# Kernel optimization log

Hardware: AMD Instinct MI355X
Metric: run time of the kernel (lower is better)

Reference implementation:

```python
import jax, jax.numpy as jnp
import numpy as np

N, DIN, H, OUT = 2048, 128, 64, 7


def setup_inputs() -> dict:
    key = jax.random.key(0)
    ks = jax.random.split(key, 24)

    def lin(k, out_d, in_d):
        kw, kb = jax.random.split(k)
        s = 1.0 / np.sqrt(in_d)
        W = jax.random.uniform(kw, (out_d, in_d), minval=-s, maxval=s, dtype=jnp.float32)
        b = jax.random.uniform(kb, (out_d,), minval=-s, maxval=s, dtype=jnp.float32)
        return W, b

    x = jax.random.normal(ks[0], (N, DIN), dtype=jnp.float32)
    A = jax.random.uniform(ks[1], (N, N), dtype=jnp.float32)
    W1, b1 = lin(ks[2], H, DIN)
    WF1, bF1 = lin(ks[3], H, H)
    WF2, bF2 = lin(ks[4], H, H)
    WT1, bT1 = lin(ks[5], H, H)
    WT2, bT2 = lin(ks[6], H, H)
    WC1, bC1 = lin(ks[7], H, H)
    WC2, bC2 = lin(ks[8], H, H)
    Wa, ba = lin(ks[9], H, H)
    q = jax.random.normal(ks[10], (H,), dtype=jnp.float32)
    W2, b2 = lin(ks[11], OUT, H)
    return dict(x=x, A=A, k=4, W1=W1, b1=b1, WF1=WF1, bF1=bF1, WF2=WF2, bF2=bF2,
                WT1=WT1, bT1=bT1, WT2=WT2, bT2=bT2, WC1=WC1, bC1=bC1, WC2=WC2,
                bC2=bC2, Wa=Wa, ba=ba, q=q, W2=W2, b2=b2)


def leaky(x):
    return jnp.where(x > 0, x, 0.1 * x)


def laplacian(A):
    # D^{-1/2} A D^{-1/2} with diagonal D of (rowsum + 1e-10)
    d = (jnp.sum(A, -1) + 1e-10) ** -0.5
    return A * d[:, None] * d[None, :]


def cos_sim(x):
    n = jnp.sqrt(jnp.sum(x * x, -1, keepdims=True))
    s = x / n + 1e-10  # note: +1e-10 AFTER the division, as in the source
    return s @ s.T


def heat(x):
    # exp(-0.5 * sum_d ((x_i - x_j)^2 + 1e-10)); gram trick, same math as
    # the [d, N, N] broadcasted version in the source.
    sq = jnp.sum(x * x, -1)
    dist = sq[:, None] + sq[None, :] - 2.0 * (x @ x.T) + x.shape[-1] * 1e-10
    return jnp.exp(-0.5 * dist)


def l2_norm_rows(x):
    m = jnp.sqrt(jnp.mean(x * x, -1)) + 1e-10
    return x / m[:, None]


def hsic(x1, x2):
    n = x1.shape[-2]
    K1 = x1 @ x1.T
    K2 = x2 @ x2.T
    Rm = jnp.eye(n, dtype=x1.dtype) - jnp.ones((n, n), dtype=x1.dtype) / n
    P = Rm @ K1 @ Rm  # [N, N]
    # mean(I * (P @ K2)) * n^2/(n-1)^2 = trace(P @ K2)/(n-1)^2; K2 symmetric
    return jnp.sum(P * K2) / (n - 1) ** 2


def gnn(z, Ad, W, b):
    return leaky((Ad @ z) @ W.T + b)


def reference(x, A, k, W1, b1, WF1, bF1, WF2, bF2, WT1, bT1, WT2, bT2,
              WC1, bC1, WC2, bC2, Wa, ba, q, W2, b2):
    h = leaky(x @ W1.T + b1)                       # [N, H]
    At = laplacian(A)
    Hh = heat(h)                                    # [N, N]
    rank = jnp.argsort(jnp.argsort(-Hh, axis=-1), axis=-1)  # double-argsort rank
    mask = (rank < k).astype(h.dtype)
    Af = laplacian(cos_sim(h) * mask)
    zf = gnn(gnn(h, Af, WF1, bF1), Af, WF2, bF2)
    zt = gnn(gnn(h, At, WT1, bT1), At, WT2, bT2)
    zcf = gnn(gnn(h, Af, WC1, bC1), Af, WC2, bC2)
    zct = gnn(gnn(h, At, WC1, bC1), At, WC2, bC2)
    Lcf = l2_norm_rows(zcf)
    Lct = l2_norm_rows(zct)
    Lc = jnp.mean((Lcf @ Lcf.T - Lct @ Lct.T) ** 2)
    Ld = hsic(zt, zct) + hsic(zf, zcf)
    zc = (zcf + zct) / 2
    z = jnp.stack([zf, zt, zc], axis=-2)            # [N, 3, H]
    a = jax.nn.softmax(jnp.tanh(z @ Wa.T + ba) @ q, axis=-1)  # [N, 3]
    zagg = jnp.einsum('nkd,nk->nd', z, a)           # [N, H]
    out = zagg @ W2.T + b2                          # [N, OUT]
    return (out, Lc, Ld)
```

## Files before the change

kernel.cpp:

```cpp
#include <hip/hip_runtime.h>
#include <stdint.h>

#define N 2048
#define DIN 128
#define H 64
#define OUTD 7
#define RS 32
#define S1 8
#define S2 8

#define Z_ZT  0
#define Z_ZCT 64
#define Z_ZF  128
#define Z_ZCF 192
#define Z_LCF 256
#define Z_LCT 320

typedef short bf16x8 __attribute__((ext_vector_type(8)));
typedef float floatx4 __attribute__((ext_vector_type(4)));

__device__ __forceinline__ float leaky(float x){ return x > 0.f ? x : 0.1f*x; }

__device__ __forceinline__ unsigned short f2bf(float f){
  unsigned int u = __float_as_uint(f);
  u = u + 0x7FFFu + ((u >> 16) & 1u);
  return (unsigned short)(u >> 16);
}

__device__ __forceinline__ float waveRedSum(float v){
  #pragma unroll
  for (int o = 32; o > 0; o >>= 1) v += __shfl_xor(v, o, 64);
  return v;
}

__device__ __forceinline__ unsigned long long shflx64(unsigned long long v, int m){
  unsigned int lo = (unsigned int)v, hi = (unsigned int)(v >> 32);
  lo = (unsigned int)__shfl_xor((int)lo, m, 64);
  hi = (unsigned int)__shfl_xor((int)hi, m, 64);
  return ((unsigned long long)hi << 32) | lo;
}

__global__ void k_prep(const float* __restrict__ A, float* __restrict__ dA,
                       unsigned short* __restrict__ Abf){
  int i = blockIdx.x;
  const float4* row = (const float4*)(A + (size_t)i * N);
  unsigned short* ob = Abf + (size_t)i * N;
  float s = 0.f;
  #pragma unroll
  for (int it = 0; it < 2; it++){
    int u = threadIdx.x + it*256;
    float4 v = row[u];
    s += v.x + v.y + v.z + v.w;
    ushort4 o;
    o.x = f2bf(v.x); o.y = f2bf(v.y); o.z = f2bf(v.z); o.w = f2bf(v.w);
    *(ushort4*)&ob[u*4] = o;
  }
  __shared__ float red[4];
  s = waveRedSum(s);
  int wid = threadIdx.x >> 6, lane = threadIdx.x & 63;
  if (lane == 0) red[wid] = s;
  __syncthreads();
  if (threadIdx.x == 0){
    float t = red[0] + red[1] + red[2] + red[3];
    dA[i] = 1.0f / sqrtf(t + 1e-10f);
  }
}

__global__ __launch_bounds__(256) void k_h(const float* __restrict__ x,
                    const float* __restrict__ W1g, const float* __restrict__ b1,
                    const float* __restrict__ dA,
                    float* __restrict__ h, unsigned short* __restrict__ hsT,
                    float* __restrict__ sq, float* __restrict__ hsum){
  __shared__ float W1t[DIN][H+1];
  __shared__ float xb[4][DIN];
  __shared__ __align__(16) unsigned short hTb[H][16];
  int tid = threadIdx.x, w = tid >> 6, t = tid & 63;
  int i0 = blockIdx.x * 16;
  for (int u = tid; u < 2048; u += 256){
    float4 g = ((const float4*)W1g)[u];
    int row = u >> 5, c0 = (u & 31) * 4;
    W1t[c0+0][row] = g.x; W1t[c0+1][row] = g.y;
    W1t[c0+2][row] = g.z; W1t[c0+3][row] = g.w;
  }
  __syncthreads();
  float bt = b1[t];
  for (int rr = 0; rr < 4; rr++){
    int i = i0 + w*4 + rr;
    xb[w][t]      = x[(size_t)i*DIN + t];
    xb[w][t + 64] = x[(size_t)i*DIN + t + 64];
    float acc = bt;
    #pragma unroll
    for (int c4 = 0; c4 < DIN/4; c4++){
      float xv[4]; *(float4*)xv = *(const float4*)&xb[w][c4*4];
      acc += xv[0]*W1t[c4*4+0][t] + xv[1]*W1t[c4*4+1][t]
           + xv[2]*W1t[c4*4+2][t] + xv[3]*W1t[c4*4+3][t];
    }
    float hv = leaky(acc);
    h[(size_t)i*H + t] = hv;
    hTb[t][w*4+rr] = f2bf(dA[i]*hv);
    float s2 = waveRedSum(hv*hv);
    float s1 = waveRedSum(hv);
    if (t == 0){ sq[i] = s2; hsum[i] = s1; }
  }
  __syncthreads();
  { int c = tid >> 2, qq = tid & 3;
    ushort4 v = *(ushort4*)&hTb[c][qq*4];
    *(ushort4*)&hsT[(size_t)c*N + i0 + qq*4] = v; }
}

__global__ __launch_bounds__(256) void k_gram(const float* __restrict__ h,
                                              float* __restrict__ DOT){
  __shared__ float at[32][132];
  __shared__ float bt[32][132];
  int bi = blockIdx.x, bj = blockIdx.y;
  int tid = threadIdx.x;
  int rg = tid >> 4, cg = tid & 15;
  float acc[8][8] = {};
  for (int kc = 0; kc < 64; kc += 32){
    for (int u = tid; u < 1024; u += 256){
      int row = u >> 3, k4 = u & 7;
      float4 v = *(const float4*)(h + (size_t)(bi*128 + row)*H + kc + k4*4);
      at[k4*4+0][row] = v.x; at[k4*4+1][row] = v.y;
      at[k4*4+2][row] = v.z; at[k4*4+3][row] = v.w;
    }
    for (int u = tid; u < 1024; u += 256){
      int row = u >> 3, k4 = u & 7;
      float4 v = *(const float4*)(h + (size_t)(bj*128 + row)*H + kc + k4*4);
      bt[k4*4+0][row] = v.x; bt[k4*4+1][row] = v.y;
      bt[k4*4+2][row] = v.z; bt[k4*4+3][row] = v.w;
    }
    __syncthreads();
    for (int k = 0; k < 32; k++){
      float a[8], b[8];
      *(float4*)&a[0] = *(const float4*)&at[k][rg*8];
      *(float4*)&a[4] = *(const float4*)&at[k][rg*8+4];
      *(float4*)&b[0] = *(const float4*)&bt[k][cg*8];
      *(float4*)&b[4] = *(const float4*)&bt[k][cg*8+4];
      #pragma unroll
      for (int ii = 0; ii < 8; ii++)
        #pragma unroll
        for (int jj = 0; jj < 8; jj++)
          acc[ii][jj] += a[ii]*b[jj];
    }
    __syncthreads();
  }
  #pragma unroll
  for (int ii = 0; ii < 8; ii++){
    int r = bi*128 + rg*8 + ii;
    float* out = DOT + (size_t)r*N + bj*128 + cg*8;
    *(float4*)(out)   = make_float4(acc[ii][0], acc[ii][1], acc[ii][2], acc[ii][3]);
    *(float4*)(out+4) = make_float4(acc[ii][4], acc[ii][5], acc[ii][6], acc[ii][7]);
  }
}

__global__ __launch_bounds__(256) void k_topk(const float* __restrict__ DOT,
      const float* __restrict__ sq, const float* __restrict__ hsum,
      int* __restrict__ nidx, float* __restrict__ ncos, float* __restrict__ df){
  int i = blockIdx.x, tid = threadIdx.x;
  __shared__ unsigned long long cand[1024];
  const float4* row = (const float4*)(DOT + (size_t)i * N);
  const float4* sq4 = (const float4*)sq;
  unsigned long long best[4] = {~0ULL, ~0ULL, ~0ULL, ~0ULL};
  #pragma unroll
  for (int blk = 0; blk < 2; blk++){
    int u = tid + blk*256;
    float4 d = row[u];
    float4 s = sq4[u];
    float kv[4] = { s.x - 2.f*d.x, s.y - 2.f*d.y, s.z - 2.f*d.z, s.w - 2.f*d.w };
    #pragma unroll
    for (int e = 0; e < 4; e++){
      unsigned int j = (unsigned int)(u*4 + e);
      unsigned int uk = __float_as_uint(kv[e]);
      uk = (uk & 0x80000000u) ? ~uk : (uk | 0x80000000u);
      unsigned long long c = ((unsigned long long)uk << 32) | j;
      if (c < best[3]){
        best[3] = c;
        unsigned long long t0;
        if (best[3] < best[2]){ t0 = best[2]; best[2] = best[3]; best[3] = t0; }
        if (best[2] < best[1]){ t0 = best[1]; best[1] = best[2]; best[2] = t0; }
        if (best[1] < best[0]){ t0 = best[0]; best[0] = best[1]; best[1] = t0; }
      }
    }
  }
  #pragma unroll
  for (int e = 0; e < 4; e++) cand[e*256 + tid] = best[e];
  __syncthreads();
  if (tid < 64){
    unsigned long long loc[16];
    #pragma unroll
    for (int e = 0; e < 16; e++) loc[e] = cand[e*64 + tid];
    unsigned long long w0=~0ULL, w1=~0ULL, w2=~0ULL, w3=~0ULL;
    #pragma unroll
    for (int r = 0; r < 4; r++){
      unsigned long long m = loc[0];
      #pragma unroll
      for (int e = 1; e < 16; e++) m = (loc[e] < m) ? loc[e] : m;
      unsigned long long g = m;
      #pragma unroll
      for (int o = 32; o > 0; o >>= 1){
        unsigned long long other = shflx64(g, o);
        if (other < g) g = other;
      }
      #pragma unroll
      for (int e = 0; e < 16; e++) if (loc[e] == g) loc[e] = ~0ULL;
      if (r == 0) w0 = g; else if (r == 1) w1 = g; else if (r == 2) w2 = g; else w3 = g;
    }
    float myc = 0.f;
    if (tid < 4){
      unsigned long long w = (tid==0) ? w0 : (tid==1) ? w1 : (tid==2) ? w2 : w3;
      unsigned int j = (unsigned int)w;
      unsigned int uk = (unsigned int)(w >> 32);
      float key = (uk & 0x80000000u) ? __uint_as_float(uk ^ 0x80000000u)
                                     : __uint_as_float(~uk);
      float sqj = sq[j];
      float dot = (sqj - key) * 0.5f;
      float hni = sqrtf(sq[i]), hnj = sqrtf(sqj);
      float cosv = dot/(hni*hnj)
                 + 1e-10f*(hsum[i]/hni + hsum[j]/hnj)
                 + 64.0f*1e-20f;
      nidx[i*4 + tid] = (int)j;
      ncos[i*4 + tid] = cosv;
      myc = cosv;
    }
    myc += __shfl_xor(myc, 1, 64);
    myc += __shfl_xor(myc, 2, 64);
    if (tid == 0) df[i] = 1.f / sqrtf(myc + 1e-10f);
  }
}

template<int BN>
__global__ __launch_bounds__(256) void k_mgemm(
    const unsigned short* __restrict__ Abf, const unsigned short* __restrict__ BtG,
    float* __restrict__ Cp, int KC){
  __shared__ __align__(16) unsigned short Asl[64][72];
  __shared__ __align__(16) unsigned short Bsl[BN][72];
  int m0 = blockIdx.x * 64, kbase = blockIdx.y * KC;
  int tid = threadIdx.x;
  int w = tid >> 6, lane = tid & 63;
  int quad = lane >> 4, ml = lane & 15;
  floatx4 acc[BN/16];
  #pragma unroll
  for (int ct = 0; ct < BN/16; ct++) acc[ct] = (floatx4){0.f,0.f,0.f,0.f};

  for (int kc = 0; kc < KC; kc += 64){
    int kb = kbase + kc;
    #pragma unroll
    for (int u = tid; u < 512; u += 256){
      int r = u >> 3, s = u & 7;
      *(uint4*)&Asl[r][s*8] = *(const uint4*)(Abf + ((size_t)(m0+r) << 11) + kb + s*8);
    }
    #pragma unroll
    for (int u = tid; u < BN*8; u += 256){
      int n = u >> 3, s = u & 7;
      *(uint4*)&Bsl[n][s*8] = *(const uint4*)(BtG + ((size_t)n << 11) + kb + s*8);
    }
    __syncthreads();
    #pragma unroll
    for (int k0 = 0; k0 < 64; k0 += 32){
      bf16x8 af = *(const bf16x8*)&Asl[16*w + ml][k0 + quad*8];
      #pragma unroll
      for (int ct = 0; ct < BN/16; ct++){
        bf16x8 bfr = *(const bf16x8*)&Bsl[16*ct + ml][k0 + quad*8];
        acc[ct] = __builtin_amdgcn_mfma_f32_16x16x32_bf16(af, bfr, acc[ct], 0, 0, 0);
      }
    }
    __syncthreads();
  }
  float* C = Cp + (size_t)blockIdx.y * (N * BN);
  #pragma unroll
  for (int ct = 0; ct < BN/16; ct++)
    #pragma unroll
    for (int r = 0; r < 4; r++){
      int row = m0 + 16*w + quad*4 + r;
      C[(size_t)row*BN + 16*ct + ml] = acc[ct][r];
    }
}

__global__ __launch_bounds__(256) void k_sumY1(const float* __restrict__ Y1p,
    const float* __restrict__ dA, unsigned short* __restrict__ Ub1){
  int idx4 = blockIdx.x*256 + threadIdx.x;
  int i = idx4 >> 4;
  float4 s = ((const float4*)Y1p)[idx4];
  #pragma unroll
  for (int p = 1; p < S1; p++){
    float4 v = ((const float4*)Y1p)[(size_t)p*(N*H/4) + idx4];
    s.x += v.x; s.y += v.y; s.z += v.z; s.w += v.w;
  }
  float d = dA[i];
  ushort4 o;
  o.x = f2bf(s.x*d); o.y = f2bf(s.y*d); o.z = f2bf(s.z*d); o.w = f2bf(s.w*d);
  ((ushort4*)Ub1)[idx4] = o;
}

__global__ __launch_bounds__(256) void k_sumY2(const float* __restrict__ Y2p,
    const float* __restrict__ dA, unsigned short* __restrict__ Ub2){
  int idx4 = blockIdx.x*256 + threadIdx.x;
  int i = idx4 >> 5;
  float4 s = ((const float4*)Y2p)[idx4];
  #pragma unroll
  for (int p = 1; p < S2; p++){
    float4 v = ((const float4*)Y2p)[(size_t)p*(N*128/4) + idx4];
    s.x += v.x; s.y += v.y; s.z += v.z; s.w += v.w;
  }
  float d = dA[i];
  ushort4 o;
  o.x = f2bf(s.x*d); o.y = f2bf(s.y*d); o.z = f2bf(s.z*d); o.w = f2bf(s.w*d);
  ((ushort4*)Ub2)[idx4] = o;
}

__global__ __launch_bounds__(256) void k_gather1(const float* __restrict__ h,
    const int* __restrict__ nidx, const float* __restrict__ ncos,
    const float* __restrict__ df, unsigned short* __restrict__ Vb1){
  int tid = threadIdx.x, w = tid >> 6, t = tid & 63;
  int i = blockIdx.x*4 + w;
  int j0 = nidx[i*4], j1 = nidx[i*4+1], j2 = nidx[i*4+2], j3 = nidx[i*4+3];
  float di = df[i];
  float w0 = ncos[i*4]  *di*df[j0];
  float w1 = ncos[i*4+1]*di*df[j1];
  float w2 = ncos[i*4+2]*di*df[j2];
  float w3 = ncos[i*4+3]*di*df[j3];
  float v = w0*h[(size_t)j0*H+t] + w1*h[(size_t)j1*H+t]
          + w2*h[(size_t)j2*H+t] + w3*h[(size_t)j3*H+t];
  Vb1[(size_t)i*H + t] = f2bf(v);
}

__global__ __launch_bounds__(256) void k_gather2(const float* __restrict__ z1f,
    const float* __restrict__ z1cf,
    const int* __restrict__ nidx, const float* __restrict__ ncos,
    const float* __restrict__ df,
    unsigned short* __restrict__ Vf2, unsigned short* __restrict__ Vc2){
  int tid = threadIdx.x, w = tid >> 6, t = tid & 63;
  int i = blockIdx.x*4 + w;
  int j0 = nidx[i*4], j1 = nidx[i*4+1], j2 = nidx[i*4+2], j3 = nidx[i*4+3];
  float di = df[i];
  float w0 = ncos[i*4]  *di*df[j0];
  float w1 = ncos[i*4+1]*di*df[j1];
  float w2 = ncos[i*4+2]*di*df[j2];
  float w3 = ncos[i*4+3]*di*df[j3];
  float vf = w0*z1f[(size_t)j0*H+t] + w1*z1f[(size_t)j1*H+t]
           + w2*z1f[(size_t)j2*H+t] + w3*z1f[(size_t)j3*H+t];
  float vc = w0*z1cf[(size_t)j0*H+t] + w1*z1cf[(size_t)j1*H+t]
           + w2*z1cf[(size_t)j2*H+t] + w3*z1cf[(size_t)j3*H+t];
  Vf2[(size_t)i*H + t] = f2bf(vf);
  Vc2[(size_t)i*H + t] = f2bf(vc);
}

__global__ __launch_bounds__(256) void k_z1m(
    const unsigned short* __restrict__ Vb1, const unsigned short* __restrict__ Ub1,
    const float* __restrict__ WF1, const float* __restrict__ WC1,
    const float* __restrict__ WT1, const float* __restrict__ bF1,
    const float* __restrict__ bC1, const float* __restrict__ bT1,
    const float* __restrict__ dA,
    float* __restrict__ z1f, float* __restrict__ z1cf,
    unsigned short* __restrict__ ZsT){
  __shared__ __align__(16) unsigned short Vs[64][72];
  __shared__ __align__(16) unsigned short Ws[64][72];
  __shared__ __align__(16) unsigned short Tb[64][72];
  __shared__ float bias[64], dAl[64];
  int p = blockIdx.y, i0 = blockIdx.x * 64, tid = threadIdx.x;
  const unsigned short* Vsrc = (p < 2) ? Vb1 : Ub1;
  const float* Wsrc = (p == 0) ? WF1 : (p == 2) ? WT1 : WC1;
  const float* bsrc = (p == 0) ? bF1 : (p == 2) ? bT1 : bC1;
  #pragma unroll
  for (int u = tid; u < 512; u += 256){
    int r = u >> 3, s = u & 7;
    *(uint4*)&Vs[r][s*8] = *(const uint4*)(Vsrc + (size_t)(i0+r)*H + s*8);
  }
  for (int u = tid; u < 1024; u += 256){
    int r = u >> 4, c4 = (u & 15)*4;
    float4 f = *(const float4*)(Wsrc + (size_t)r*H + c4);
    Ws[r][c4+0] = f2bf(f.x); Ws[r][c4+1] = f2bf(f.y);
    Ws[r][c4+2] = f2bf(f.z); Ws[r][c4+3] = f2bf(f.w);
  }
  if (tid < 64){ bias[tid] = bsrc[tid]; dAl[tid] = dA[i0 + tid]; }
  __syncthreads();
  int w = tid >> 6, lane = tid & 63, quad = lane >> 4, ml = lane & 15;
  floatx4 acc[4];
  #pragma unroll
  for (int ct = 0; ct < 4; ct++) acc[ct] = (floatx4){0.f,0.f,0.f,0.f};
  #pragma unroll
  for (int k0 = 0; k0 < 64; k0 += 32){
    bf16x8 af = *(const bf16x8*)&Vs[16*w + ml][k0 + quad*8];
    #pragma unroll
    for (int ct = 0; ct < 4; ct++){
      bf16x8 bfr = *(const bf16x8*)&Ws[16*ct + ml][k0 + quad*8];
      acc[ct] = __builtin_amdgcn_mfma_f32_16x16x32_bf16(af, bfr, acc[ct], 0, 0, 0);
    }
  }
  if (p < 2){
    float* dst = (p == 0) ? z1f : z1cf;
    #pragma unroll
    for (int ct = 0; ct < 4; ct++){
      int col = 16*ct + ml;
      #pragma unroll
      for (int r = 0; r < 4; r++){
        int row = 16*w + quad*4 + r;
        dst[(size_t)(i0+row)*H + col] = leaky(acc[ct][r] + bias[col]);
      }
    }
  } else {
    #pragma unroll
    for (int ct = 0; ct < 4; ct++){
      int col = 16*ct + ml;
      #pragma unroll
      for (int r = 0; r < 4; r++){
        int row = 16*w + quad*4 + r;
        Tb[col][row] = f2bf(dAl[row] * leaky(acc[ct][r] + bias[col]));
      }
    }
    __syncthreads();
    int zb = (p == 2) ? 0 : 64;
    #pragma unroll
    for (int u = tid; u < 512; u += 256){
      int c = u >> 3, s = u & 7;
      *(uint4*)&ZsT[(size_t)(zb + c)*N + i0 + s*8] = *(uint4*)&Tb[c][s*8];
    }
  }
}

__global__ __launch_bounds__(256) void k_z2m(
    const unsigned short* __restrict__ Vf2, const unsigned short* __restrict__ Vc2,
    const unsigned short* __restrict__ Ub2,
    const float* __restrict__ WF2, const float* __restrict__ WC2,
    const float* __restrict__ WT2, const float* __restrict__ bF2,
    const float* __restrict__ bC2, const float* __restrict__ bT2,
    float* __restrict__ Z6){
  __shared__ __align__(16) unsigned short Vs[64][72];
  __shared__ __align__(16) unsigned short Ws[64][72];
  __shared__ float bias[64];
  int p = blockIdx.y, i0 = blockIdx.x * 64, tid = threadIdx.x;
  const unsigned short* vptr = (p == 0) ? Vf2 : (p == 1) ? Vc2 : Ub2;
  int vstride = (p < 2) ? 64 : 128;
  int voff = (p == 3) ? 64 : 0;
  const float* Wsrc = (p == 0) ? WF2 : (p == 2) ? WT2 : WC2;
  const float* bsrc = (p == 0) ? bF2 : (p == 2) ? bT2 : bC2;
  #pragma unroll
  for (int u = tid; u < 512; u += 256){
    int r = u >> 3, s = u & 7;
    *(uint4*)&Vs[r][s*8] = *(const uint4*)(vptr + (size_t)(i0+r)*vstride + voff + s*8);
  }
  for (int u = tid; u < 1024; u += 256){
    int r = u >> 4, c4 = (u & 15)*4;
    float4 f = *(const float4*)(Wsrc + (size_t)r*H + c4);
    Ws[r][c4+0] = f2bf(f.x); Ws[r][c4+1] = f2bf(f.y);
    Ws[r][c4+2] = f2bf(f.z); Ws[r][c4+3] = f2bf(f.w);
  }
  if (tid < 64) bias[tid] = bsrc[tid];
  __syncthreads();
  int w = tid >> 6, lane = tid & 63, quad = lane >> 4, ml = lane & 15;
  floatx4 acc[4];
  #pragma unroll
  for (int ct = 0; ct < 4; ct++) acc[ct] = (floatx4){0.f,0.f,0.f,0.f};
  #pragma unroll
  for (int k0 = 0; k0 < 64; k0 += 32){
    bf16x8 af = *(const bf16x8*)&Vs[16*w + ml][k0 + quad*8];
    #pragma unroll
    for (int ct = 0; ct < 4; ct++){
      bf16x8 bfr = *(const bf16x8*)&Ws[16*ct + ml][k0 + quad*8];
      acc[ct] = __builtin_amdgcn_mfma_f32_16x16x32_bf16(af, bfr, acc[ct], 0, 0, 0);
    }
  }
  int zoff = (p == 0) ? Z_ZF : (p == 1) ? Z_ZCF : (p == 2) ? Z_ZT : Z_ZCT;
  float val[4][4];
  #pragma unroll
  for (int ct = 0; ct < 4; ct++){
    int col = 16*ct + ml;
    #pragma unroll
    for (int r = 0; r < 4; r++){
      val[ct][r] = leaky(acc[ct][r] + bias[col]);
      int row = 16*w + quad*4 + r;
      Z6[(size_t)(i0+row)*384 + zoff + col] = val[ct][r];
    }
  }
  if (p == 1 || p == 3){
    int loff = (p == 1) ? Z_LCF : Z_LCT;
    #pragma unroll
    for (int r = 0; r < 4; r++){
      float s = val[0][r]*val[0][r] + val[1][r]*val[1][r]
              + val[2][r]*val[2][r] + val[3][r]*val[3][r];
      s += __shfl_xor(s, 1, 64); s += __shfl_xor(s, 2, 64);
      s += __shfl_xor(s, 4, 64); s += __shfl_xor(s, 8, 64);
      float m = sqrtf(s*(1.f/64.f)) + 1e-10f;
      int row = 16*w + quad*4 + r;
      #pragma unroll
      for (int ct = 0; ct < 4; ct++)
        Z6[(size_t)(i0+row)*384 + loff + 16*ct + ml] = val[ct][r]/m;
    }
  }
}

__global__ __launch_bounds__(256) void k_att(const float* __restrict__ Z6,
    const float* __restrict__ Wag, const float* __restrict__ ba,
    const float* __restrict__ q, const float* __restrict__ W2g,
    const float* __restrict__ b2, float* __restrict__ out){
  __shared__ float Wal[64][65];
  __shared__ float W2l[448];
  __shared__ float zbuf[4][3][66];
  __shared__ float zagg[4][66];
  int tid = threadIdx.x, w = tid >> 6, t = tid & 63;
  for (int u = tid; u < 1024; u += 256){
    int r = u >> 4, c4 = (u & 15)*4;
    float4 f = ((const float4*)Wag)[u];
    Wal[r][c4+0]=f.x; Wal[r][c4+1]=f.y; Wal[r][c4+2]=f.z; Wal[r][c4+3]=f.w;
  }
  if (tid < 112) *(float4*)&W2l[tid*4] = ((const float4*)W2g)[tid];
  __syncthreads();
  int i = blockIdx.x*4 + w;
  const float* zr = Z6 + (size_t)i*384;
  float zf = zr[Z_ZF + t], zt = zr[Z_ZT + t];
  float zc = 0.5f*(zr[Z_ZCF + t] + zr[Z_ZCT + t]);
  zbuf[w][0][t] = zf; zbuf[w][1][t] = zt; zbuf[w][2][t] = zc;
  __syncthreads();
  float bav = ba[t], qv = q[t];
  float e[3];
  #pragma unroll
  for (int k = 0; k < 3; k++){
    float S = bav;
    #pragma unroll 8
    for (int c = 0; c < 64; c++) S += zbuf[w][k][c] * Wal[t][c];
    e[k] = waveRedSum(tanhf(S)*qv);
  }
  float mx = fmaxf(e[0], fmaxf(e[1], e[2]));
  float x0 = expf(e[0]-mx), x1 = expf(e[1]-mx), x2 = expf(e[2]-mx);
  float inv = 1.f/(x0+x1+x2);
  zagg[w][t] = x0*inv*zf + x1*inv*zt + x2*inv*zc;
  __syncthreads();
  if (t < OUTD){
    float acc = b2[t];
    #pragma unroll 8
    for (int c = 0; c < 64; c++) acc += zagg[w][c]*W2l[t*64 + c];
    out[(size_t)i*OUTD + t] = acc;
  }
}

__global__ __launch_bounds__(256) void k_reduce(const float* __restrict__ Z6,
                                                float* __restrict__ redP,
                                                float* __restrict__ colP){
  __shared__ float sa[64][68];
  __shared__ float sb[64][68];
  int p = blockIdx.x >> 5;
  int s = blockIdx.x & 31;
  int tid = threadIdx.x;
  const int aoffT[5] = {Z_ZT,  Z_ZF,  Z_LCF, Z_LCF, Z_LCT};
  const int boffT[5] = {Z_ZCT, Z_ZCF, Z_LCF, Z_LCT, Z_LCT};
  int aoff = aoffT[p], boff = boffT[p];
  int r0 = s * 64;
  {
    int row = tid >> 4, c4 = (tid & 15) * 4;
    #pragma unroll
    for (int rr = 0; rr < 64; rr += 16){
      const float* zr = Z6 + (size_t)(r0 + row + rr) * 384;
      *(float4*)&sa[row + rr][c4] = *(const float4*)&zr[aoff + c4];
      *(float4*)&sb[row + rr][c4] = *(const float4*)&zr[boff + c4];
    }
  }
  __syncthreads();
  int rg = tid >> 4, cg = tid & 15;
  float acc[4][4] = {};
  #pragma unroll 8
  for (int k = 0; k < 64; k++){
    float a[4], b[4];
    *(float4*)a = *(const float4*)&sa[k][rg*4];
    *(float4*)b = *(const float4*)&sb[k][cg*4];
    #pragma unroll
    for (int ii = 0; ii < 4; ii++)
      #pragma unroll
      for (int jj = 0; jj < 4; jj++)
        acc[ii][jj] += a[ii]*b[jj];
  }
  float* rp = redP + (size_t)blockIdx.x * 4096;
  #pragma unroll
  for (int ii = 0; ii < 4; ii++)
    *(float4*)&rp[(rg*4+ii)*64 + cg*4] =
      make_float4(acc[ii][0], acc[ii][1], acc[ii][2], acc[ii][3]);
  if (p < 2 && tid < 128){
    int t = tid & 63;
    float csum = 0.f;
    if (tid < 64){
      #pragma unroll 16
      for (int r = 0; r < 64; r++) csum += sa[r][t];
    } else {
      #pragma unroll 16
      for (int r = 0; r < 64; r++) csum += sb[r][t];
    }
    colP[((size_t)p*RS + s)*128 + tid] = csum;
  }
}

__global__ void k_combine(const float* __restrict__ redP,
                          const float* __restrict__ colP,
                          float* __restrict__ red){
  int idx = blockIdx.x*256 + threadIdx.x;
  if (idx < 20480){
    int p = idx >> 12, i = idx & 4095;
    float sum = 0.f;
    #pragma unroll 8
    for (int s = 0; s < RS; s++) sum += redP[((size_t)p*RS + s)*4096 + i];
    red[idx] = sum;
  } else if (idx < 20736){
    int j = idx - 20480;
    int p = j >> 7, rem = j & 127;
    float sum = 0.f;
    #pragma unroll 8
    for (int s = 0; s < RS; s++) sum += colP[((size_t)p*RS + s)*128 + rem];
    red[idx] = sum;
  }
}

__global__ void k_final(const float* __restrict__ red, float* __restrict__ out2){
  int tid = threadIdx.x;
  const float* Stc = red;
  const float* Sfc = red + 4096;
  const float* Cff = red + 8192;
  const float* Cft = red + 12288;
  const float* Ctt = red + 16384;
  const float* cst = red + 20480;
  const float* csct= red + 20544;
  const float* csf = red + 20608;
  const float* cscf= red + 20672;
  float sCff=0, sCft=0, sCtt=0, sM1=0, sM2=0;
  for (int u = tid*16; u < tid*16+16; u++){
    int d = u >> 6, e = u & 63;
    float m1 = Stc[u] - cst[d]*csct[e]*(1.f/2048.f);
    float m2 = Sfc[u] - csf[d]*cscf[e]*(1.f/2048.f);
    sM1 += m1*m1; sM2 += m2*m2;
    float cf = Cff[u], cx = Cft[u], ct = Ctt[u];
    sCff += cf*cf; sCft += cx*cx; sCtt += ct*ct;
  }
  __shared__ float rd[5][4];
  sCff = waveRedSum(sCff); sCft = waveRedSum(sCft); sCtt = waveRedSum(sCtt);
  sM1 = waveRedSum(sM1);   sM2 = waveRedSum(sM2);
  int w = tid >> 6, lane = tid & 63;
  if (lane == 0){ rd[0][w]=sCff; rd[1][w]=sCft; rd[2][w]=sCtt; rd[3][w]=sM1; rd[4][w]=sM2; }
  __syncthreads();
  if (tid == 0){
    float A0 = rd[0][0]+rd[0][1]+rd[0][2]+rd[0][3];
    float A1 = rd[1][0]+rd[1][1]+rd[1][2]+rd[1][3];
    float A2 = rd[2][0]+rd[2][1]+rd[2][2]+rd[2][3];
    float M1 = rd[3][0]+rd[3][1]+rd[3][2]+rd[3][3];
    float M2 = rd[4][0]+rd[4][1]+rd[4][2]+rd[4][3];
    out2[0] = (A0 - 2.f*A1 + A2) * (1.f/(2048.f*2048.f));
    out2[1] = (M1 + M2) * (1.f/(2047.f*2047.f));
  }
}

extern "C" void kernel_launch(void* const* d_in, const int* in_sizes, int n_in,
                              void* d_out, int out_size, void* d_ws, size_t ws_size,
                              hipStream_t stream) {
  const float* x   = (const float*)d_in[0];
  const float* A   = (const float*)d_in[1];
  const float* W1  = (const float*)d_in[3];
  const float* b1  = (const float*)d_in[4];
  const float* WF1 = (const float*)d_in[5];
  const float* bF1 = (const float*)d_in[6];
  const float* WF2 = (const float*)d_in[7];
  const float* bF2 = (const float*)d_in[8];
  const float* WT1 = (const float*)d_in[9];
  const float* bT1 = (const float*)d_in[10];
  const float* WT2 = (const float*)d_in[11];
  const float* bT2 = (const float*)d_in[12];
  const float* WC1 = (const float*)d_in[13];
  const float* bC1 = (const float*)d_in[14];
  const float* WC2 = (const float*)d_in[15];
  const float* bC2 = (const float*)d_in[16];
  const float* Wa  = (const float*)d_in[17];
  const float* ba  = (const float*)d_in[18];
  const float* q   = (const float*)d_in[19];
  const float* W2  = (const float*)d_in[20];
  const float* b2  = (const float*)d_in[21];
  float* out = (float*)d_out;

  float* W = (float*)d_ws;
  float* h_   = W;
  float* dA   = h_  + N*H;
  float* sq   = dA  + N;
  float* hsum = sq  + N;
  float* df   = hsum+ N;
  int*   nidx = (int*)(df + N);
  float* ncos = (float*)(nidx + N*4);
  float* red  = ncos + N*4;
  float* DOT  = red + 20736;
  float* Z6   = DOT + (size_t)N*N;
  float* Y1p  = Z6  + (size_t)N*384;
  float* Y2p  = Y1p + (size_t)S1*N*H;
  float* z1f  = Y2p + (size_t)S2*N*128;
  float* z1cf = z1f + N*H;
  float* redP = z1cf+ N*H;
  float* colP = redP+ 655360;
  unsigned short* Abf = (unsigned short*)(colP + 8192);
  unsigned short* hsT = Abf + (size_t)N*N;
  unsigned short* ZsT = hsT + (size_t)H*N;
  unsigned short* Vb1 = ZsT + (size_t)128*N;
  unsigned short* Ub1 = Vb1 + (size_t)N*H;
  unsigned short* Vf2 = Ub1 + (size_t)N*H;
  unsigned short* Vc2 = Vf2 + (size_t)N*H;
  unsigned short* Ub2 = Vc2 + (size_t)N*H;

  k_prep<<<N, 256, 0, stream>>>(A, dA, Abf);
  k_h<<<128, 256, 0, stream>>>(x, W1, b1, dA, h_, hsT, sq, hsum);
  k_gram<<<dim3(16,16), 256, 0, stream>>>(h_, DOT);
  k_topk<<<N, 256, 0, stream>>>(DOT, sq, hsum, nidx, ncos, df);
  k_gather1<<<512, 256, 0, stream>>>(h_, nidx, ncos, df, Vb1);

  k_mgemm<64><<<dim3(32,S1), 256, 0, stream>>>(Abf, hsT, Y1p, N/S1);
  k_sumY1<<<128, 256, 0, stream>>>(Y1p, dA, Ub1);
  k_z1m<<<dim3(32,4), 256, 0, stream>>>(Vb1, Ub1, WF1, WC1, WT1, bF1, bC1, bT1,
                                        dA, z1f, z1cf, ZsT);
  k_mgemm<128><<<dim3(32,S2), 256, 0, stream>>>(Abf, ZsT, Y2p, N/S2);
  k_sumY2<<<256, 256, 0, stream>>>(Y2p, dA, Ub2);
  k_gather2<<<512, 256, 0, stream>>>(z1f, z1cf, nidx, ncos, df, Vf2, Vc2);
  k_z2m<<<dim3(32,4), 256, 0, stream>>>(Vf2, Vc2, Ub2, WF2, WC2, WT2,
                                        bF2, bC2, bT2, Z6);
  k_att<<<512, 256, 0, stream>>>(Z6, Wa, ba, q, W2, b2, out);
  k_reduce<<<5*RS, 256, 0, stream>>>(Z6, redP, colP);
  k_combine<<<81, 256, 0, stream>>>(redP, colP, red);
  k_final<<<1, 256, 0, stream>>>(red, out + (size_t)N*OUTD);
}
```

Before: 204.1 us.

## Split-bf16 MFMA gram, wave-per-row topk, fuse gathers and split-K sums into z kernels

The fp32 FMA gram kernel is replaced by an MFMA version that splits h into bf16 hi/lo parts and uses three products to keep near-fp32 accuracy. Top-k is restructured so each wave handles one row with a shuffle-based merge, removing the shared-memory candidate stage. The separate gather and split-K reduction kernels are folded into the z1m/z2m GEMM prologues, which removes four launches and their intermediate bf16 buffers. The risks are that the hi/lo approximation could change top-k neighbour choices on near ties, and that the gather in k_z1m now reads bf16 h instead of fp32.

```diff
diff --git a/kernel.cpp b/kernel.cpp
--- a/kernel.cpp
+++ b/kernel.cpp
@@ -27,6 +27,10 @@
   return (unsigned short)(u >> 16);
 }
 
+__device__ __forceinline__ float bf2f(unsigned short u){
+  return __uint_as_float((unsigned int)u << 16);
+}
+
 __device__ __forceinline__ float waveRedSum(float v){
   #pragma unroll
   for (int o = 32; o > 0; o >>= 1) v += __shfl_xor(v, o, 64);
@@ -69,7 +73,9 @@
 __global__ __launch_bounds__(256) void k_h(const float* __restrict__ x,
                     const float* __restrict__ W1g, const float* __restrict__ b1,
                     const float* __restrict__ dA,
-                    float* __restrict__ h, unsigned short* __restrict__ hsT,
+                    unsigned short* __restrict__ hb_hi,
+                    unsigned short* __restrict__ hb_lo,
+                    unsigned short* __restrict__ hsT,
                     float* __restrict__ sq, float* __restrict__ hsum){
   __shared__ float W1t[DIN][H+1];
   __shared__ float xb[4][DIN];
@@ -96,7 +102,9 @@
            + xv[2]*W1t[c4*4+2][t] + xv[3]*W1t[c4*4+3][t];
     }
     float hv = leaky(acc);
-    h[(size_t)i*H + t] = hv;
+    unsigned short hi = f2bf(hv);
+    hb_hi[(size_t)i*H + t] = hi;
+    hb_lo[(size_t)i*H + t] = f2bf(hv - bf2f(hi));
     hTb[t][w*4+rr] = f2bf(dA[i]*hv);
     float s2 = waveRedSum(hv*hv);
     float s1 = waveRedSum(hv);
@@ -108,62 +116,63 @@
     *(ushort4*)&hsT[(size_t)c*N + i0 + qq*4] = v; }
 }
 
-__global__ __launch_bounds__(256) void k_gram(const float* __restrict__ h,
-                                              float* __restrict__ DOT){
-  __shared__ float at[32][132];
-  __shared__ float bt[32][132];
-  int bi = blockIdx.x, bj = blockIdx.y;
-  int tid = threadIdx.x;
-  int rg = tid >> 4, cg = tid & 15;
-  float acc[8][8] = {};
-  for (int kc = 0; kc < 64; kc += 32){
-    for (int u = tid; u < 1024; u += 256){
-      int row = u >> 3, k4 = u & 7;
-      float4 v = *(const float4*)(h + (size_t)(bi*128 + row)*H + kc + k4*4);
-      at[k4*4+0][row] = v.x; at[k4*4+1][row] = v.y;
-      at[k4*4+2][row] = v.z; at[k4*4+3][row] = v.w;
-    }
-    for (int u = tid; u < 1024; u += 256){
-      int row = u >> 3, k4 = u & 7;
-      float4 v = *(const float4*)(h + (size_t)(bj*128 + row)*H + kc + k4*4);
-      bt[k4*4+0][row] = v.x; bt[k4*4+1][row] = v.y;
-      bt[k4*4+2][row] = v.z; bt[k4*4+3][row] = v.w;
-    }
-    __syncthreads();
-    for (int k = 0; k < 32; k++){
-      float a[8], b[8];
-      *(float4*)&a[0] = *(const float4*)&at[k][rg*8];
-      *(float4*)&a[4] = *(const float4*)&at[k][rg*8+4];
-      *(float4*)&b[0] = *(const float4*)&bt[k][cg*8];
-      *(float4*)&b[4] = *(const float4*)&bt[k][cg*8+4];
-      #pragma unroll
-      for (int ii = 0; ii < 8; ii++)
-        #pragma unroll
-        for (int jj = 0; jj < 8; jj++)
-          acc[ii][jj] += a[ii]*b[jj];
-    }
-    __syncthreads();
-  }
-  #pragma unroll
-  for (int ii = 0; ii < 8; ii++){
-    int r = bi*128 + rg*8 + ii;
-    float* out = DOT + (size_t)r*N + bj*128 + cg*8;
-    *(float4*)(out)   = make_float4(acc[ii][0], acc[ii][1], acc[ii][2], acc[ii][3]);
-    *(float4*)(out+4) = make_float4(acc[ii][4], acc[ii][5], acc[ii][6], acc[ii][7]);
-  }
+__global__ __launch_bounds__(256) void k_gram2(
+    const unsigned short* __restrict__ Hhi, const unsigned short* __restrict__ Hlo,
+    float* __restrict__ DOT){
+  __shared__ __align__(16) unsigned short Bh[128][72];
+  __shared__ __align__(16) unsigned short Bl[128][72];
+  int bi = blockIdx.x, bj = blockIdx.y, tid = threadIdx.x;
+  for (int u = tid; u < 1024; u += 256){
+    int r = u >> 3, s = u & 7;
+    *(uint4*)&Bh[r][s*8] = *(const uint4*)(Hhi + (size_t)(bj*128+r)*H + s*8);
+    *(uint4*)&Bl[r][s*8] = *(const uint4*)(Hlo + (size_t)(bj*128+r)*H + s*8);
+  }
+  __syncthreads();
+  int w = tid >> 6, lane = tid & 63, quad = lane >> 4, ml = lane & 15;
+  floatx4 acc[2][8];
+  #pragma unroll
+  for (int rt = 0; rt < 2; rt++)
+    #pragma unroll
+    for (int ct = 0; ct < 8; ct++) acc[rt][ct] = (floatx4){0.f,0.f,0.f,0.f};
+  #pragma unroll
+  for (int rt = 0; rt < 2; rt++){
+    int arow = bi*128 + (2*w + rt)*16 + ml;
+    #pragma unroll
+    for (int k0 = 0; k0 < 64; k0 += 32){
+      bf16x8 ah = *(const bf16x8*)(Hhi + (size_t)arow*H + k0 + quad*8);
+      bf16x8 al = *(const bf16x8*)(Hlo + (size_t)arow*H + k0 + quad*8);
+      #pragma unroll
+      for (int ct = 0; ct < 8; ct++){
+        bf16x8 bh = *(const bf16x8*)&Bh[ct*16 + ml][k0 + quad*8];
+        bf16x8 bl = *(const bf16x8*)&Bl[ct*16 + ml][k0 + quad*8];
+        acc[rt][ct] = __builtin_amdgcn_mfma_f32_16x16x32_bf16(ah, bh, acc[rt][ct], 0,0,0);
+        acc[rt][ct] = __builtin_amdgcn_mfma_f32_16x16x32_bf16(ah, bl, acc[rt][ct], 0,0,0);
+        acc[rt][ct] = __builtin_amdgcn_mfma_f32_16x16x32_bf16(al, bh, acc[rt][ct], 0,0,0);
+      }
+    }
+  }
+  #pragma unroll
+  for (int rt = 0; rt < 2; rt++)
+    #pragma unroll
+    for (int ct = 0; ct < 8; ct++)
+      #pragma unroll
+      for (int r = 0; r < 4; r++){
+        int row = bi*128 + (2*w+rt)*16 + quad*4 + r;
+        DOT[(size_t)row*N + bj*128 + ct*16 + ml] = acc[rt][ct][r];
+      }
 }
 
 __global__ __launch_bounds__(256) void k_topk(const float* __restrict__ DOT,
       const float* __restrict__ sq, const float* __restrict__ hsum,
       int* __restrict__ nidx, float* __restrict__ ncos, float* __restrict__ df){
-  int i = blockIdx.x, tid = threadIdx.x;
-  __shared__ unsigned long long cand[1024];
+  int tid = threadIdx.x, w = tid >> 6, lane = tid & 63;
+  int i = blockIdx.x*4 + w;
   const float4* row = (const float4*)(DOT + (size_t)i * N);
   const float4* sq4 = (const float4*)sq;
   unsigned long long best[4] = {~0ULL, ~0ULL, ~0ULL, ~0ULL};
   #pragma unroll
-  for (int blk = 0; blk < 2; blk++){
-    int u = tid + blk*256;
+  for (int it = 0; it < 8; it++){
+    int u = it*64 + lane;
     float4 d = row[u];
     float4 s = sq4[u];
     float kv[4] = { s.x - 2.f*d.x, s.y - 2.f*d.y, s.z - 2.f*d.z, s.w - 2.f*d.w };
@@ -182,50 +191,41 @@
       }
     }
   }
-  #pragma unroll
-  for (int e = 0; e < 4; e++) cand[e*256 + tid] = best[e];
-  __syncthreads();
-  if (tid < 64){
-    unsigned long long loc[16];
-    #pragma unroll
-    for (int e = 0; e < 16; e++) loc[e] = cand[e*64 + tid];
-    unsigned long long w0=~0ULL, w1=~0ULL, w2=~0ULL, w3=~0ULL;
-    #pragma unroll
-    for (int r = 0; r < 4; r++){
-      unsigned long long m = loc[0];
-      #pragma unroll
-      for (int e = 1; e < 16; e++) m = (loc[e] < m) ? loc[e] : m;
-      unsigned long long g = m;
-      #pragma unroll
-      for (int o = 32; o > 0; o >>= 1){
-        unsigned long long other = shflx64(g, o);
-        if (other < g) g = other;
-      }
-      #pragma unroll
-      for (int e = 0; e < 16; e++) if (loc[e] == g) loc[e] = ~0ULL;
-      if (r == 0) w0 = g; else if (r == 1) w1 = g; else if (r == 2) w2 = g; else w3 = g;
-    }
-    float myc = 0.f;
-    if (tid < 4){
-      unsigned long long w = (tid==0) ? w0 : (tid==1) ? w1 : (tid==2) ? w2 : w3;
-      unsigned int j = (unsigned int)w;
-      unsigned int uk = (unsigned int)(w >> 32);
-      float key = (uk & 0x80000000u) ? __uint_as_float(uk ^ 0x80000000u)
-                                     : __uint_as_float(~uk);
-      float sqj = sq[j];
-      float dot = (sqj - key) * 0.5f;
-      float hni = sqrtf(sq[i]), hnj = sqrtf(sqj);
-      float cosv = dot/(hni*hnj)
-                 + 1e-10f*(hsum[i]/hni + hsum[j]/hnj)
-                 + 64.0f*1e-20f;
-      nidx[i*4 + tid] = (int)j;
-      ncos[i*4 + tid] = cosv;
-      myc = cosv;
-    }
-    myc += __shfl_xor(myc, 1, 64);
-    myc += __shfl_xor(myc, 2, 64);
-    if (tid == 0) df[i] = 1.f / sqrtf(myc + 1e-10f);
-  }
+  unsigned long long win[4];
+  #pragma unroll
+  for (int r = 0; r < 4; r++){
+    unsigned long long m = best[0];
+    #pragma unroll
+    for (int o = 1; o < 64; o <<= 1){
+      unsigned long long other = shflx64(m, o);
+      if (other < m) m = other;
+    }
+    win[r] = m;
+    if      (best[0]==m){best[0]=best[1];best[1]=best[2];best[2]=best[3];best[3]=~0ULL;}
+    else if (best[1]==m){best[1]=best[2];best[2]=best[3];best[3]=~0ULL;}
+    else if (best[2]==m){best[2]=best[3];best[3]=~0ULL;}
+    else if (best[3]==m){best[3]=~0ULL;}
+  }
+  float myc = 0.f;
+  if (lane < 4){
+    unsigned long long wv = win[lane];
+    unsigned int j = (unsigned int)wv;
+    unsigned int uk = (unsigned int)(wv >> 32);
+    float key = (uk & 0x80000000u) ? __uint_as_float(uk ^ 0x80000000u)
+                                   : __uint_as_float(~uk);
+    float sqj = sq[j];
+    float dot = (sqj - key) * 0.5f;
+    float hni = sqrtf(sq[i]), hnj = sqrtf(sqj);
+    float cosv = dot/(hni*hnj)
+               + 1e-10f*(hsum[i]/hni + hsum[j]/hnj)
+               + 64.0f*1e-20f;
+    nidx[i*4 + lane] = (int)j;
+    ncos[i*4 + lane] = cosv;
+    myc = cosv;
+  }
+  myc += __shfl_xor(myc, 1, 64);
+  myc += __shfl_xor(myc, 2, 64);
+  if (lane == 0) df[i] = 1.f / sqrtf(myc + 1e-10f);
 }
 
 template<int BN>
@@ -276,81 +276,14 @@
     }
 }
 
-__global__ __launch_bounds__(256) void k_sumY1(const float* __restrict__ Y1p,
-    const float* __restrict__ dA, unsigned short* __restrict__ Ub1){
-  int idx4 = blockIdx.x*256 + threadIdx.x;
-  int i = idx4 >> 4;
-  float4 s = ((const float4*)Y1p)[idx4];
-  #pragma unroll
-  for (int p = 1; p < S1; p++){
-    float4 v = ((const float4*)Y1p)[(size_t)p*(N*H/4) + idx4];
-    s.x += v.x; s.y += v.y; s.z += v.z; s.w += v.w;
-  }
-  float d = dA[i];
-  ushort4 o;
-  o.x = f2bf(s.x*d); o.y = f2bf(s.y*d); o.z = f2bf(s.z*d); o.w = f2bf(s.w*d);
-  ((ushort4*)Ub1)[idx4] = o;
-}
-
-__global__ __launch_bounds__(256) void k_sumY2(const float* __restrict__ Y2p,
-    const float* __restrict__ dA, unsigned short* __restrict__ Ub2){
-  int idx4 = blockIdx.x*256 + threadIdx.x;
-  int i = idx4 >> 5;
-  float4 s = ((const float4*)Y2p)[idx4];
-  #pragma unroll
-  for (int p = 1; p < S2; p++){
-    float4 v = ((const float4*)Y2p)[(size_t)p*(N*128/4) + idx4];
-    s.x += v.x; s.y += v.y; s.z += v.z; s.w += v.w;
-  }
-  float d = dA[i];
-  ushort4 o;
-  o.x = f2bf(s.x*d); o.y = f2bf(s.y*d); o.z = f2bf(s.z*d); o.w = f2bf(s.w*d);
-  ((ushort4*)Ub2)[idx4] = o;
-}
-
-__global__ __launch_bounds__(256) void k_gather1(const float* __restrict__ h,
-    const int* __restrict__ nidx, const float* __restrict__ ncos,
-    const float* __restrict__ df, unsigned short* __restrict__ Vb1){
-  int tid = threadIdx.x, w = tid >> 6, t = tid & 63;
-  int i = blockIdx.x*4 + w;
-  int j0 = nidx[i*4], j1 = nidx[i*4+1], j2 = nidx[i*4+2], j3 = nidx[i*4+3];
-  float di = df[i];
-  float w0 = ncos[i*4]  *di*df[j0];
-  float w1 = ncos[i*4+1]*di*df[j1];
-  float w2 = ncos[i*4+2]*di*df[j2];
-  float w3 = ncos[i*4+3]*di*df[j3];
-  float v = w0*h[(size_t)j0*H+t] + w1*h[(size_t)j1*H+t]
-          + w2*h[(size_t)j2*H+t] + w3*h[(size_t)j3*H+t];
-  Vb1[(size_t)i*H + t] = f2bf(v);
-}
-
-__global__ __launch_bounds__(256) void k_gather2(const float* __restrict__ z1f,
-    const float* __restrict__ z1cf,
+__global__ __launch_bounds__(256) void k_z1m(
+    const unsigned short* __restrict__ hb,
     const int* __restrict__ nidx, const float* __restrict__ ncos,
     const float* __restrict__ df,
-    unsigned short* __restrict__ Vf2, unsigned short* __restrict__ Vc2){
-  int tid = threadIdx.x, w = tid >> 6, t = tid & 63;
-  int i = blockIdx.x*4 + w;
-  int j0 = nidx[i*4], j1 = nidx[i*4+1], j2 = nidx[i*4+2], j3 = nidx[i*4+3];
-  float di = df[i];
-  float w0 = ncos[i*4]  *di*df[j0];
-  float w1 = ncos[i*4+1]*di*df[j1];
-  float w2 = ncos[i*4+2]*di*df[j2];
-  float w3 = ncos[i*4+3]*di*df[j3];
-  float vf = w0*z1f[(size_t)j0*H+t] + w1*z1f[(size_t)j1*H+t]
-           + w2*z1f[(size_t)j2*H+t] + w3*z1f[(size_t)j3*H+t];
-  float vc = w0*z1cf[(size_t)j0*H+t] + w1*z1cf[(size_t)j1*H+t]
-           + w2*z1cf[(size_t)j2*H+t] + w3*z1cf[(size_t)j3*H+t];
-  Vf2[(size_t)i*H + t] = f2bf(vf);
-  Vc2[(size_t)i*H + t] = f2bf(vc);
-}
-
-__global__ __launch_bounds__(256) void k_z1m(
-    const unsigned short* __restrict__ Vb1, const unsigned short* __restrict__ Ub1,
+    const float* __restrict__ Y1p, const float* __restrict__ dA,
     const float* __restrict__ WF1, const float* __restrict__ WC1,
     const float* __restrict__ WT1, const float* __restrict__ bF1,
     const float* __restrict__ bC1, const float* __restrict__ bT1,
-    const float* __restrict__ dA,
     float* __restrict__ z1f, float* __restrict__ z1cf,
     unsigned short* __restrict__ ZsT){
   __shared__ __align__(16) unsigned short Vs[64][72];
@@ -358,14 +291,9 @@
   __shared__ __align__(16) unsigned short Tb[64][72];
   __shared__ float bias[64], dAl[64];
   int p = blockIdx.y, i0 = blockIdx.x * 64, tid = threadIdx.x;
-  const unsigned short* Vsrc = (p < 2) ? Vb1 : Ub1;
+  int w = tid >> 6, lane = tid & 63;
   const float* Wsrc = (p == 0) ? WF1 : (p == 2) ? WT1 : WC1;
   const float* bsrc = (p == 0) ? bF1 : (p == 2) ? bT1 : bC1;
-  #pragma unroll
-  for (int u = tid; u < 512; u += 256){
-    int r = u >> 3, s = u & 7;
-    *(uint4*)&Vs[r][s*8] = *(const uint4*)(Vsrc + (size_t)(i0+r)*H + s*8);
-  }
   for (int u = tid; u < 1024; u += 256){
     int r = u >> 4, c4 = (u & 15)*4;
     float4 f = *(const float4*)(Wsrc + (size_t)r*H + c4);
@@ -373,8 +301,36 @@
     Ws[r][c4+2] = f2bf(f.z); Ws[r][c4+3] = f2bf(f.w);
   }
   if (tid < 64){ bias[tid] = bsrc[tid]; dAl[tid] = dA[i0 + tid]; }
-  __syncthreads();
-  int w = tid >> 6, lane = tid & 63, quad = lane >> 4, ml = lane & 15;
+  if (p < 2){
+    for (int rr = 0; rr < 16; rr++){
+      int r = w*16 + rr, i = i0 + r;
+      int j0 = nidx[i*4], j1 = nidx[i*4+1], j2 = nidx[i*4+2], j3 = nidx[i*4+3];
+      float di = df[i];
+      float w0 = ncos[i*4]  *di*df[j0];
+      float w1 = ncos[i*4+1]*di*df[j1];
+      float w2 = ncos[i*4+2]*di*df[j2];
+      float w3 = ncos[i*4+3]*di*df[j3];
+      float v = w0*bf2f(hb[(size_t)j0*H+lane]) + w1*bf2f(hb[(size_t)j1*H+lane])
+              + w2*bf2f(hb[(size_t)j2*H+lane]) + w3*bf2f(hb[(size_t)j3*H+lane]);
+      Vs[r][lane] = f2bf(v);
+    }
+  } else {
+    for (int u = tid; u < 1024; u += 256){
+      int r = u >> 4, k4 = u & 15;
+      const float* base = Y1p + (size_t)(i0 + r)*H + k4*4;
+      float4 s = *(const float4*)base;
+      #pragma unroll
+      for (int pp = 1; pp < S1; pp++){
+        float4 v2 = *(const float4*)(base + (size_t)pp*N*H);
+        s.x += v2.x; s.y += v2.y; s.z += v2.z; s.w += v2.w;
+      }
+      float d = dA[i0 + r];
+      Vs[r][k4*4+0] = f2bf(s.x*d); Vs[r][k4*4+1] = f2bf(s.y*d);
+      Vs[r][k4*4+2] = f2bf(s.z*d); Vs[r][k4*4+3] = f2bf(s.w*d);
+    }
+  }
+  __syncthreads();
+  int quad = lane >> 4, ml = lane & 15;
   floatx4 acc[4];
   #pragma unroll
   for (int ct = 0; ct < 4; ct++) acc[ct] = (floatx4){0.f,0.f,0.f,0.f};
@@ -419,8 +375,10 @@
 }
 
 __global__ __launch_bounds__(256) void k_z2m(
-    const unsigned short* __restrict__ Vf2, const unsigned short* __restrict__ Vc2,
-    const unsigned short* __restrict__ Ub2,
+    const float* __restrict__ z1f, const float* __restrict__ z1cf,
+    const int* __restrict__ nidx, const float* __restrict__ ncos,
+    const float* __restrict__ df,
+    const float* __restrict__ Y2p, const float* __restrict__ dA,
     const float* __restrict__ WF2, const float* __restrict__ WC2,
     const float* __restrict__ WT2, const float* __restrict__ bF2,
     const float* __restrict__ bC2, const float* __restrict__ bT2,
@@ -429,16 +387,9 @@
   __shared__ __align__(16) unsigned short Ws[64][72];
   __shared__ float bias[64];
   int p = blockIdx.y, i0 = blockIdx.x * 64, tid = threadIdx.x;
-  const unsigned short* vptr = (p == 0) ? Vf2 : (p == 1) ? Vc2 : Ub2;
-  int vstride = (p < 2) ? 64 : 128;
-  int voff = (p == 3) ? 64 : 0;
+  int w = tid >> 6, lane = tid & 63;
   const float* Wsrc = (p == 0) ? WF2 : (p == 2) ? WT2 : WC2;
   const float* bsrc = (p == 0) ? bF2 : (p == 2) ? bT2 : bC2;
-  #pragma unroll
-  for (int u = tid; u < 512; u += 256){
-    int r = u >> 3, s = u & 7;
-    *(uint4*)&Vs[r][s*8] = *(const uint4*)(vptr + (size_t)(i0+r)*vstride + voff + s*8);
-  }
   for (int u = tid; u < 1024; u += 256){
     int r = u >> 4, c4 = (u & 15)*4;
     float4 f = *(const float4*)(Wsrc + (size_t)r*H + c4);
@@ -446,8 +397,38 @@
     Ws[r][c4+2] = f2bf(f.z); Ws[r][c4+3] = f2bf(f.w);
   }
   if (tid < 64) bias[tid] = bsrc[tid];
-  __syncthreads();
-  int w = tid >> 6, lane = tid & 63, quad = lane >> 4, ml = lane & 15;
+  if (p < 2){
+    const float* src = (p == 0) ? z1f : z1cf;
+    for (int rr = 0; rr < 16; rr++){
+      int r = w*16 + rr, i = i0 + r;
+      int j0 = nidx[i*4], j1 = nidx[i*4+1], j2 = nidx[i*4+2], j3 = nidx[i*4+3];
+      float di = df[i];
+      float w0 = ncos[i*4]  *di*df[j0];
+      float w1 = ncos[i*4+1]*di*df[j1];
+      float w2 = ncos[i*4+2]*di*df[j2];
+      float w3 = ncos[i*4+3]*di*df[j3];
+      float v = w0*src[(size_t)j0*H+lane] + w1*src[(size_t)j1*H+lane]
+              + w2*src[(size_t)j2*H+lane] + w3*src[(size_t)j3*H+lane];
+      Vs[r][lane] = f2bf(v);
+    }
+  } else {
+    int off = (p == 2) ? 0 : 64;
+    for (int u = tid; u < 1024; u += 256){
+      int r = u >> 4, k4 = u & 15;
+      const float* base = Y2p + (size_t)(i0 + r)*128 + off + k4*4;
+      float4 s = *(const float4*)base;
+      #pragma unroll
+      for (int pp = 1; pp < S2; pp++){
+        float4 v2 = *(const float4*)(base + (size_t)pp*N*128);
+        s.x += v2.x; s.y += v2.y; s.z += v2.z; s.w += v2.w;
+      }
+      float d = dA[i0 + r];
+      Vs[r][k4*4+0] = f2bf(s.x*d); Vs[r][k4*4+1] = f2bf(s.y*d);
+      Vs[r][k4*4+2] = f2bf(s.z*d); Vs[r][k4*4+3] = f2bf(s.w*d);
+    }
+  }
+  __syncthreads();
+  int quad = lane >> 4, ml = lane & 15;
   floatx4 acc[4];
   #pragma unroll
   for (int ct = 0; ct < 4; ct++) acc[ct] = (floatx4){0.f,0.f,0.f,0.f};
@@ -671,8 +652,7 @@
   float* out = (float*)d_out;
 
   float* W = (float*)d_ws;
-  float* h_   = W;
-  float* dA   = h_  + N*H;
+  float* dA   = W;
   float* sq   = dA  + N;
   float* hsum = sq  + N;
   float* df   = hsum+ N;
@@ -687,30 +667,24 @@
   float* z1cf = z1f + N*H;
   float* redP = z1cf+ N*H;
   float* colP = redP+ 655360;
-  unsigned short* Abf = (unsigned short*)(colP + 8192);
-  unsigned short* hsT = Abf + (size_t)N*N;
-  unsigned short* ZsT = hsT + (size_t)H*N;
-  unsigned short* Vb1 = ZsT + (size_t)128*N;
-  unsigned short* Ub1 = Vb1 + (size_t)N*H;
-  unsigned short* Vf2 = Ub1 + (size_t)N*H;
-  unsigned short* Vc2 = Vf2 + (size_t)N*H;
-  unsigned short* Ub2 = Vc2 + (size_t)N*H;
+  unsigned short* Abf  = (unsigned short*)(colP + 8192);
+  unsigned short* hsT  = Abf + (size_t)N*N;
+  unsigned short* ZsT  = hsT + (size_t)H*N;
+  unsigned short* hbHi = ZsT + (size_t)128*N;
+  unsigned short* hbLo = hbHi + (size_t)N*H;
 
   k_prep<<<N, 256, 0, stream>>>(A, dA, Abf);
-  k_h<<<128, 256, 0, stream>>>(x, W1, b1, dA, h_, hsT, sq, hsum);
-  k_gram<<<dim3(16,16), 256, 0, stream>>>(h_, DOT);
-  k_topk<<<N, 256, 0, stream>>>(DOT, sq, hsum, nidx, ncos, df);
-  k_gather1<<<512, 256, 0, stream>>>(h_, nidx, ncos, df, Vb1);
+  k_h<<<128, 256, 0, stream>>>(x, W1, b1, dA, hbHi, hbLo, hsT, sq, hsum);
+  k_gram2<<<dim3(16,16), 256, 0, stream>>>(hbHi, hbLo, DOT);
+  k_topk<<<512, 256, 0, stream>>>(DOT, sq, hsum, nidx, ncos, df);
 
   k_mgemm<64><<<dim3(32,S1), 256, 0, stream>>>(Abf, hsT, Y1p, N/S1);
-  k_sumY1<<<128, 256, 0, stream>>>(Y1p, dA, Ub1);
-  k_z1m<<<dim3(32,4), 256, 0, stream>>>(Vb1, Ub1, WF1, WC1, WT1, bF1, bC1, bT1,
-                                        dA, z1f, z1cf, ZsT);
+  k_z1m<<<dim3(32,4), 256, 0, stream>>>(hbHi, nidx, ncos, df, Y1p, dA,
+                                        WF1, WC1, WT1, bF1, bC1, bT1,
+                                        z1f, z1cf, ZsT);
   k_mgemm<128><<<dim3(32,S2), 256, 0, stream>>>(Abf, ZsT, Y2p, N/S2);
-  k_sumY2<<<256, 256, 0, stream>>>(Y2p, dA, Ub2);
-  k_gather2<<<512, 256, 0, stream>>>(z1f, z1cf, nidx, ncos, df, Vf2, Vc2);
-  k_z2m<<<dim3(32,4), 256, 0, stream>>>(Vf2, Vc2, Ub2, WF2, WC2, WT2,
-                                        bF2, bC2, bT2, Z6);
+  k_z2m<<<dim3(32,4), 256, 0, stream>>>(z1f, z1cf, nidx, ncos, df, Y2p, dA,
+                                        WF2, WC2, WT2, bF2, bC2, bT2, Z6);
   k_att<<<512, 256, 0, stream>>>(Z6, Wa, ba, q, W2, b2, out);
   k_reduce<<<5*RS, 256, 0, stream>>>(Z6, redP, colP);
   k_combine<<<81, 256, 0, stream>>>(redP, colP, red);
```

Measured after the change: 197.2 us. 3.4% less time.
